# Optimization experiments

Measured on AMD Instinct MI355X. Metric: run time of the kernel, lower is better.

Reference implementation:

```python
import jax, jax.numpy as jnp
import numpy as np

B = 2
E = [16384, 32768, 65536, 131072]
CONVS = [256, 128, 64, 32, 8]


def mesh_conv(x, gemm, W, b):
    # x: (B, C, E); gemm: (E, 4) neighbor edge indices; W: (Cout, Cin, 5)
    n = x[:, :, gemm]  # (B, C, E, 4) irregular gather over mesh topology
    f1, f2, f3, f4 = n[..., 0], n[..., 1], n[..., 2], n[..., 3]
    # MeshCNN symmetric functions over the 4 gemm neighbors
    G = jnp.stack([x, f1 + f3, f2 + f4, jnp.abs(f1 - f3), jnp.abs(f2 - f4)], axis=-1)  # (B,C,E,5)
    return jnp.einsum('bces,ocs->boe', G, W) + b[None, :, None]


def inorm(x, eps=1e-5):
    # InstanceNorm2d, affine=False: normalize per (sample, channel) over edge dim
    m = jnp.mean(x, axis=2, keepdims=True)
    v = jnp.var(x, axis=2, keepdims=True)
    return (x - m) * jax.lax.rsqrt(v + eps)


def setup_inputs() -> dict:
    key = jax.random.key(0)
    ks = iter(jax.random.split(key, 64))
    inp = {}
    inp['fe'] = jax.random.normal(next(ks), (B, CONVS[0], E[0]), jnp.float32)
    for i in range(3):
        inp[f'skip{i}'] = jax.random.normal(next(ks), (B, CONVS[i + 1], E[i + 1]), jnp.float32)
    for r in range(4):
        inp[f'gemm{r}'] = jax.random.randint(next(ks), (E[r], 4), 0, E[r], jnp.int32)
    for i in range(3):
        inp[f'unpool{i}'] = jax.random.randint(next(ks), (E[i + 1],), 0, E[i], jnp.int32)

    def mk(cout, cin, name):
        inp[f'W{name}'] = jax.random.normal(next(ks), (cout, cin, 5), jnp.float32) * (1.0 / np.sqrt(5.0 * cin))
        inp[f'b{name}'] = jnp.zeros((cout,), jnp.float32)

    for i in range(3):
        mk(CONVS[i + 1], CONVS[i], f'up{i}')
        mk(CONVS[i + 1], CONVS[i + 1], f'c{i}')
    mk(CONVS[4], CONVS[3], 'upf')
    mk(CONVS[4], CONVS[4], 'cf')
    return inp


def reference(fe, skip0, skip1, skip2, gemm0, gemm1, gemm2, gemm3,
              unpool0, unpool1, unpool2,
              Wup0, bup0, Wc0, bc0, Wup1, bup1, Wc1, bc1, Wup2, bup2, Wc2, bc2,
              Wupf, bupf, Wcf, bcf):
    gemms = [gemm0, gemm1, gemm2, gemm3]
    unpools = [unpool0, unpool1, unpool2]
    skips = [skip0, skip1, skip2]
    Wups = [Wup0, Wup1, Wup2]
    bups = [bup0, bup1, bup2]
    Wcs = [Wc0, Wc1, Wc2]
    bcs = [bc0, bc1, bc2]
    x = fe
    for i in range(3):  # fixed small loop over decoder stages
        x1 = mesh_conv(x, gemms[i], Wups[i], bups[i])      # up_conv at coarse res
        x1 = x1[:, :, unpools[i]]                          # MeshUnpool: copy to fine edges
        x1 = x1 + skips[i]                                 # transfer_data skip add
        x1 = mesh_conv(x1, gemms[i + 1], Wcs[i], bcs[i])   # conv1 at fine res
        x = jax.nn.relu(inorm(x1))                         # InstanceNorm + ReLU (blocks=0)
    # final UpConv: no unroll, no skip
    x1 = mesh_conv(x, gemms[3], Wupf, bupf)
    x1 = mesh_conv(x1, gemms[3], Wcf, bcf)
    return jax.nn.relu(inorm(x1))
```

## Files before the change

kernel.cpp:

```cpp
#include <hip/hip_runtime.h>
#include <hip/hip_bf16.h>
#include <cstdint>
#include <cstddef>


typedef short s16x8 __attribute__((ext_vector_type(8)));
typedef float f32x4 __attribute__((ext_vector_type(4)));

__device__ __forceinline__ float bfbits2f(unsigned short u) {
    unsigned int x = ((unsigned int)u) << 16;
    float f; __builtin_memcpy(&f, &x, sizeof(f)); return f;
}
__device__ __forceinline__ unsigned short f2bfbits(float f) {
    __hip_bfloat16 h = __float2bfloat16(f);
    unsigned short u; __builtin_memcpy(&u, &h, sizeof(u)); return u;
}

__global__ __launch_bounds__(256) void k_transpose_in(
    const float* __restrict__ in, unsigned short* __restrict__ out, int C, int E)
{
    __shared__ float tile[64][65];
    const int e0 = blockIdx.x * 64;
    const int c0 = blockIdx.y * 64;
    const int b  = blockIdx.z;
    const float* inb = in + (size_t)b * C * E;
    const int l = threadIdx.x % 64;
    const int g = threadIdx.x / 64;
#pragma unroll
    for (int i = 0; i < 16; ++i) {
        const int c = i * 4 + g;
        tile[c][l] = inb[(size_t)(c0 + c) * E + e0 + l];
    }
    __syncthreads();
    unsigned short* outb = out + (size_t)b * E * C;
#pragma unroll
    for (int i = 0; i < 16; ++i) {
        const int e = i * 4 + g;
        outb[(size_t)(e0 + e) * C + c0 + l] = f2bfbits(tile[l][e]);
    }
}

__global__ __launch_bounds__(256) void k_prep_b(
    const float* __restrict__ W, unsigned short* __restrict__ Bp, int C, int O)
{
    const int p = blockIdx.x * 256 + threadIdx.x;
    const int total = 5 * C * O;
    if (p >= total) return;
    const int j = p & 7;
    const int t = p >> 3;
    const int o = t % O;
    const int kk = t / O;
    const int k = kk * 8 + j;
    const int s = k / C;
    const int c = k - s * C;
    Bp[p] = f2bfbits(W[((size_t)o * C + c) * 5 + s]);
}

__global__ __launch_bounds__(256) void k_prep_w(
    const float* __restrict__ W, float* __restrict__ Wt, int C, int O)
{
    const int idx = blockIdx.x * 256 + threadIdx.x;
    const int total = C * 5 * O;
    if (idx >= total) return;
    const int k = idx / O;
    const int o = idx % O;
    const int c = k / 5;
    const int s = k - 5 * c;
    Wt[idx] = W[((size_t)o * C + c) * 5 + s];
}

template<int C, int O>
__global__ __launch_bounds__(256) void k_conv_mfma(
    const unsigned short* __restrict__ x, const int* __restrict__ gm,
    const unsigned short* __restrict__ Bp, const float* __restrict__ bias,
    unsigned short* __restrict__ out, int E)
{
    constexpr int NT  = O / 16;
    constexpr int ITS = C / 32;
    static_assert(C % 32 == 0 && O % 16 == 0, "bad cfg");
    const int tid  = threadIdx.x;
    const int wave = tid >> 6;
    const int lane = tid & 63;
    const int m    = lane & 15;
    const int kq   = lane >> 4;
    const int b    = blockIdx.y;
    const int e    = blockIdx.x * 64 + wave * 16 + m;
    const unsigned short* xb = x + (size_t)b * E * C;

    const int4 gi = *reinterpret_cast<const int4*>(gm + 4 * (size_t)e);
    const unsigned short* p0  = xb + (size_t)e * C;
    const unsigned short* pf1 = xb + (size_t)gi.x * C;
    const unsigned short* pf2 = xb + (size_t)gi.y * C;
    const unsigned short* pf3 = xb + (size_t)gi.z * C;
    const unsigned short* pf4 = xb + (size_t)gi.w * C;

    const s16x8* Bp8 = reinterpret_cast<const s16x8*>(Bp);

    f32x4 acc[NT];
#pragma unroll
    for (int nt = 0; nt < NT; ++nt) acc[nt] = (f32x4){0.f, 0.f, 0.f, 0.f};

#pragma unroll
    for (int s = 0; s < 5; ++s) {
        const unsigned short* pa = (s == 0) ? p0 : ((s == 1 || s == 3) ? pf1 : pf2);
        const unsigned short* pb = (s == 0) ? p0 : ((s == 1 || s == 3) ? pf3 : pf4);
        for (int it = 0; it < ITS; ++it) {
            const int c0 = it * 32 + kq * 8;
            s16x8 afrag;
            if (s == 0) {
                afrag = *reinterpret_cast<const s16x8*>(pa + c0);
            } else {
                const s16x8 av = *reinterpret_cast<const s16x8*>(pa + c0);
                const s16x8 bv = *reinterpret_cast<const s16x8*>(pb + c0);
#pragma unroll
                for (int j = 0; j < 8; ++j) {
                    const float fa = bfbits2f((unsigned short)av[j]);
                    const float fb = bfbits2f((unsigned short)bv[j]);
                    const float t = (s < 3) ? (fa + fb) : fabsf(fa - fb);
                    afrag[j] = (short)f2bfbits(t);
                }
            }
            const int kk = s * (C / 8) + it * 4 + kq;
#pragma unroll
            for (int nt = 0; nt < NT; ++nt) {
                const s16x8 bfrag = Bp8[(size_t)kk * O + nt * 16 + m];
                acc[nt] = __builtin_amdgcn_mfma_f32_16x16x32_bf16(afrag, bfrag, acc[nt], 0, 0, 0);
            }
        }
    }

    const int ebase = blockIdx.x * 64 + wave * 16 + kq * 4;
#pragma unroll
    for (int nt = 0; nt < NT; ++nt) {
        const int o = nt * 16 + m;
        const float bo = bias[o];
#pragma unroll
        for (int r = 0; r < 4; ++r) {
            out[((size_t)b * E + (ebase + r)) * O + o] = f2bfbits(acc[nt][r] + bo);
        }
    }
}

template<int C, int O, int R_O, int R_E>
__global__ __launch_bounds__(256) void k_conv_small(
    const unsigned short* __restrict__ x, const int* __restrict__ gm,
    const float* __restrict__ Wt, const float* __restrict__ bias,
    unsigned short* __restrict__ out, int E)
{
    constexpr int OG = O / R_O;
    constexpr int EG = 256 / OG;
    constexpr int TILE_E = EG * R_E;
    static_assert(O % R_O == 0 && 256 % OG == 0, "bad cfg");
    const int tid = threadIdx.x;
    const int og  = tid % OG;
    const int eg  = tid / OG;
    const int b   = blockIdx.y;
    const int e0  = blockIdx.x * TILE_E + eg * R_E;
    const int o0  = og * R_O;
    const unsigned short* xb = x + (size_t)b * E * C;

    const unsigned short* rp[R_E][5];
#pragma unroll
    for (int j = 0; j < R_E; ++j) {
        const int e = e0 + j;
        const int4 gi = *reinterpret_cast<const int4*>(gm + 4 * (size_t)e);
        rp[j][0] = xb + (size_t)e * C;
        rp[j][1] = xb + (size_t)gi.x * C;
        rp[j][2] = xb + (size_t)gi.y * C;
        rp[j][3] = xb + (size_t)gi.z * C;
        rp[j][4] = xb + (size_t)gi.w * C;
    }

    float acc[R_E][R_O];
#pragma unroll
    for (int j = 0; j < R_E; ++j)
#pragma unroll
        for (int r = 0; r < R_O; ++r) acc[j][r] = 0.f;

    for (int c = 0; c < C; c += 4) {
        float xv[R_E][5][4];
#pragma unroll
        for (int j = 0; j < R_E; ++j)
#pragma unroll
            for (int k = 0; k < 5; ++k) {
                const ushort4 raw = *reinterpret_cast<const ushort4*>(rp[j][k] + c);
                xv[j][k][0] = bfbits2f(raw.x);
                xv[j][k][1] = bfbits2f(raw.y);
                xv[j][k][2] = bfbits2f(raw.z);
                xv[j][k][3] = bfbits2f(raw.w);
            }
#pragma unroll
        for (int cc = 0; cc < 4; ++cc) {
            float gv[R_E][5];
#pragma unroll
            for (int j = 0; j < R_E; ++j) {
                const float x0 = xv[j][0][cc];
                const float f1 = xv[j][1][cc];
                const float f2 = xv[j][2][cc];
                const float f3 = xv[j][3][cc];
                const float f4 = xv[j][4][cc];
                gv[j][0] = x0;
                gv[j][1] = f1 + f3;
                gv[j][2] = f2 + f4;
                gv[j][3] = fabsf(f1 - f3);
                gv[j][4] = fabsf(f2 - f4);
            }
            const float* wbase = Wt + ((size_t)(c + cc) * 5) * O + o0;
#pragma unroll
            for (int s = 0; s < 5; ++s) {
                const float4 wv = *reinterpret_cast<const float4*>(wbase + (size_t)s * O);
#pragma unroll
                for (int j = 0; j < R_E; ++j) {
                    acc[j][0] += gv[j][s] * wv.x;
                    acc[j][1] += gv[j][s] * wv.y;
                    acc[j][2] += gv[j][s] * wv.z;
                    acc[j][3] += gv[j][s] * wv.w;
                }
            }
        }
    }

#pragma unroll
    for (int j = 0; j < R_E; ++j) {
        ushort4 v;
        v.x = f2bfbits(acc[j][0] + bias[o0 + 0]);
        v.y = f2bfbits(acc[j][1] + bias[o0 + 1]);
        v.z = f2bfbits(acc[j][2] + bias[o0 + 2]);
        v.w = f2bfbits(acc[j][3] + bias[o0 + 3]);
        *reinterpret_cast<ushort4*>(out + ((size_t)b * E + (e0 + j)) * O + o0) = v;
    }
}

template<int O>
__global__ __launch_bounds__(256) void k_unpool_skip(
    const unsigned short* __restrict__ y, const int* __restrict__ up,
    const float* __restrict__ skip, unsigned short* __restrict__ out,
    int Ein, int Eout)
{
    const int b = blockIdx.y;
    const int idx = blockIdx.x * 256 + threadIdx.x;
    const int e = idx / O;
    const int o = idx % O;
    const int u = up[e];
    const float v = bfbits2f(y[((size_t)b * Ein + u) * O + o])
                  + skip[((size_t)b * O + o) * Eout + e];
    out[((size_t)b * Eout + e) * O + o] = f2bfbits(v);
}

template<int C>
__global__ __launch_bounds__(256) void k_stats(
    const unsigned short* __restrict__ x, float* __restrict__ stats, int E)
{
    constexpr int J = 256 / C;
    __shared__ float ssum[256];
    __shared__ float ssq[256];
    const int tid = threadIdx.x;
    const int c = tid % C;
    const int j = tid / C;
    const int b = blockIdx.y;
    const unsigned short* xb = x + ((size_t)b * E + (size_t)blockIdx.x * 256) * C;
    float s = 0.f, q = 0.f;
    for (int e = j; e < 256; e += J) {
        const float v = bfbits2f(xb[(size_t)e * C + c]);
        s += v; q += v * v;
    }
    ssum[tid] = s; ssq[tid] = q;
    __syncthreads();
    for (int st = 128; st >= C; st >>= 1) {
        if (tid < st) { ssum[tid] += ssum[tid + st]; ssq[tid] += ssq[tid + st]; }
        __syncthreads();
    }
    if (tid < C) {
        atomicAdd(&stats[((size_t)b * C + c) * 2], ssum[tid]);
        atomicAdd(&stats[((size_t)b * C + c) * 2 + 1], ssq[tid]);
    }
}

__global__ __launch_bounds__(256) void k_scale(
    const float* __restrict__ stats, float* __restrict__ ss, int BC, float invE)
{
    const int t = threadIdx.x;
    if (t < BC) {
        const float sum = stats[t * 2];
        const float sq  = stats[t * 2 + 1];
        const float m   = sum * invE;
        const float var = fmaxf(sq * invE - m * m, 0.f);
        const float sc  = rsqrtf(var + 1e-5f);
        ss[t * 2] = sc;
        ss[t * 2 + 1] = -m * sc;
    }
}

template<int C>
__global__ __launch_bounds__(256) void k_norm_relu(
    unsigned short* __restrict__ x, const float* __restrict__ ss, int E)
{
    const int b = blockIdx.y;
    const size_t idx = (size_t)blockIdx.x * 256 + threadIdx.x;
    const int c = (int)(idx % C);
    const float sc = ss[((size_t)b * C + c) * 2];
    const float sh = ss[((size_t)b * C + c) * 2 + 1];
    unsigned short* p = x + (size_t)b * E * C + idx;
    *p = f2bfbits(fmaxf(bfbits2f(*p) * sc + sh, 0.f));
}

__global__ __launch_bounds__(256) void k_final_out(
    const unsigned short* __restrict__ z, const float* __restrict__ ss,
    float* __restrict__ out, int E)
{
    const int b = blockIdx.y;
    const int idx = blockIdx.x * 256 + threadIdx.x;
    const int o = idx / E;
    const int e = idx % E;
    const float sc = ss[((size_t)b * 8 + o) * 2];
    const float sh = ss[((size_t)b * 8 + o) * 2 + 1];
    const float v = bfbits2f(z[((size_t)b * E + e) * 8 + o]) * sc + sh;
    out[(size_t)b * 8 * E + idx] = fmaxf(v, 0.f);
}

extern "C" void kernel_launch(void* const* d_in, const int* in_sizes, int n_in,
                              void* d_out, int out_size, void* d_ws, size_t ws_size,
                              hipStream_t stream)
{
    (void)in_sizes; (void)n_in; (void)out_size; (void)ws_size;

    const float* fe = (const float*)d_in[0];
    const int* gemm0 = (const int*)d_in[4];
    const int* gemm1 = (const int*)d_in[5];
    const int* gemm2 = (const int*)d_in[6];
    const int* gemm3 = (const int*)d_in[7];
    const int* up0 = (const int*)d_in[8];
    const int* up1 = (const int*)d_in[9];
    const int* up2 = (const int*)d_in[10];
    const float* bup0 = (const float*)d_in[12];
    const float* bc0  = (const float*)d_in[14];
    const float* bup1 = (const float*)d_in[16];
    const float* bc1  = (const float*)d_in[18];
    const float* bup2 = (const float*)d_in[20];
    const float* bc2  = (const float*)d_in[22];
    const float* bupf = (const float*)d_in[24];
    const float* bcf  = (const float*)d_in[26];

    unsigned short* wsb = (unsigned short*)d_ws;
    const size_t NP = 8388608;
    unsigned short* P0 = wsb;
    unsigned short* P1 = wsb + NP;
    unsigned short* P2 = wsb + 2 * NP;
    unsigned short* Bp_up0 = wsb + 3 * NP;
    unsigned short* Bp_c0  = Bp_up0 + 163840;
    unsigned short* Bp_up1 = Bp_c0  + 81920;
    unsigned short* Bp_c1  = Bp_up1 + 40960;
    unsigned short* Bp_up2 = Bp_c1  + 20480;
    unsigned short* Bp_c2  = Bp_up2 + 10240;
    float* fls    = (float*)(Bp_c2 + 5120);
    float* wt_upf = fls;
    float* wt_cf  = wt_upf + 1280;
    float* stats0 = wt_cf  + 320;
    float* stats1 = stats0 + 512;
    float* stats2 = stats1 + 256;
    float* stats3 = stats2 + 128;
    float* ss0    = stats3 + 32;
    float* ss1    = ss0 + 512;
    float* ss2    = ss1 + 256;
    float* ss3    = ss2 + 128;

    hipMemsetAsync(stats0, 0, 928 * sizeof(float), stream);

    const dim3 blk(256);

    k_transpose_in<<<dim3(16384 / 64, 256 / 64, 2), blk, 0, stream>>>(fe, P0, 256, 16384);

    k_prep_b<<<dim3(163840 / 256), blk, 0, stream>>>((const float*)d_in[11], Bp_up0, 256, 128);
    k_prep_b<<<dim3(81920 / 256),  blk, 0, stream>>>((const float*)d_in[13], Bp_c0, 128, 128);
    k_prep_b<<<dim3(40960 / 256),  blk, 0, stream>>>((const float*)d_in[15], Bp_up1, 128, 64);
    k_prep_b<<<dim3(20480 / 256),  blk, 0, stream>>>((const float*)d_in[17], Bp_c1, 64, 64);
    k_prep_b<<<dim3(10240 / 256),  blk, 0, stream>>>((const float*)d_in[19], Bp_up2, 64, 32);
    k_prep_b<<<dim3(5120 / 256),   blk, 0, stream>>>((const float*)d_in[21], Bp_c2, 32, 32);
    k_prep_w<<<dim3((1280 + 255) / 256), blk, 0, stream>>>((const float*)d_in[23], wt_upf, 32, 8);
    k_prep_w<<<dim3((320 + 255) / 256),  blk, 0, stream>>>((const float*)d_in[25], wt_cf, 8, 8);

    k_conv_mfma<256, 128><<<dim3(16384 / 64, 2), blk, 0, stream>>>(P0, gemm0, Bp_up0, bup0, P1, 16384);
    k_unpool_skip<128><<<dim3(32768 * 128 / 256, 2), blk, 0, stream>>>(P1, up0, (const float*)d_in[1], P2, 16384, 32768);
    k_conv_mfma<128, 128><<<dim3(32768 / 64, 2), blk, 0, stream>>>(P2, gemm1, Bp_c0, bc0, P0, 32768);
    k_stats<128><<<dim3(32768 / 256, 2), blk, 0, stream>>>(P0, stats0, 32768);
    k_scale<<<dim3(1), blk, 0, stream>>>(stats0, ss0, 256, 1.f / 32768.f);
    k_norm_relu<128><<<dim3(32768 * 128 / 256, 2), blk, 0, stream>>>(P0, ss0, 32768);

    k_conv_mfma<128, 64><<<dim3(32768 / 64, 2), blk, 0, stream>>>(P0, gemm1, Bp_up1, bup1, P1, 32768);
    k_unpool_skip<64><<<dim3(65536 * 64 / 256, 2), blk, 0, stream>>>(P1, up1, (const float*)d_in[2], P2, 32768, 65536);
    k_conv_mfma<64, 64><<<dim3(65536 / 64, 2), blk, 0, stream>>>(P2, gemm2, Bp_c1, bc1, P0, 65536);
    k_stats<64><<<dim3(65536 / 256, 2), blk, 0, stream>>>(P0, stats1, 65536);
    k_scale<<<dim3(1), blk, 0, stream>>>(stats1, ss1, 128, 1.f / 65536.f);
    k_norm_relu<64><<<dim3(65536 * 64 / 256, 2), blk, 0, stream>>>(P0, ss1, 65536);

    k_conv_mfma<64, 32><<<dim3(65536 / 64, 2), blk, 0, stream>>>(P0, gemm2, Bp_up2, bup2, P1, 65536);
    k_unpool_skip<32><<<dim3(131072 * 32 / 256, 2), blk, 0, stream>>>(P1, up2, (const float*)d_in[3], P2, 65536, 131072);
    k_conv_mfma<32, 32><<<dim3(131072 / 64, 2), blk, 0, stream>>>(P2, gemm3, Bp_c2, bc2, P0, 131072);
    k_stats<32><<<dim3(131072 / 256, 2), blk, 0, stream>>>(P0, stats2, 131072);
    k_scale<<<dim3(1), blk, 0, stream>>>(stats2, ss2, 64, 1.f / 131072.f);
    k_norm_relu<32><<<dim3(131072 * 32 / 256, 2), blk, 0, stream>>>(P0, ss2, 131072);

    k_conv_small<32, 8, 4, 2><<<dim3(131072 / 256, 2), blk, 0, stream>>>(P0, gemm3, wt_upf, bupf, P1, 131072);
    k_conv_small<8, 8, 4, 2><<<dim3(131072 / 256, 2), blk, 0, stream>>>(P1, gemm3, wt_cf, bcf, P2, 131072);
    k_stats<8><<<dim3(131072 / 256, 2), blk, 0, stream>>>(P2, stats3, 131072);
    k_scale<<<dim3(1), blk, 0, stream>>>(stats3, ss3, 16, 1.f / 131072.f);
    k_final_out<<<dim3(8 * 131072 / 256, 2), blk, 0, stream>>>(P2, ss3, (float*)d_out, 131072);
}
```

Before: 801.4 us.

## Fuse instance-norm stats into conv epilogues and vectorize unpool and norm kernels

Per-channel sum and sum-of-squares for instance norm are now accumulated in the conv epilogues (shuffles, shared memory, then atomics), which removes the separate stats kernels that re-read each conv output. The unpool+skip kernel now stages the channel-major skip tile through shared memory for coalesced float4 loads and writes ushort4, and norm_relu handles 8 bf16 values per thread. The small 8-output conv is rewritten so each thread owns one edge with all outputs and uses 16-byte gathers. Statistics are computed from fp32 pre-rounding values rather than the stored bf16, and atomic ordering makes them nondeterministic.

```diff
diff --git a/kernel.cpp b/kernel.cpp
--- a/kernel.cpp
+++ b/kernel.cpp
@@ -5,6 +5,7 @@
 
 
 typedef short s16x8 __attribute__((ext_vector_type(8)));
+typedef unsigned short u16x8 __attribute__((ext_vector_type(8)));
 typedef float f32x4 __attribute__((ext_vector_type(4)));
 
 __device__ __forceinline__ float bfbits2f(unsigned short u) {
@@ -69,11 +70,11 @@
     Wt[idx] = W[((size_t)o * C + c) * 5 + s];
 }
 
-template<int C, int O>
+template<int C, int O, bool STATS>
 __global__ __launch_bounds__(256) void k_conv_mfma(
     const unsigned short* __restrict__ x, const int* __restrict__ gm,
     const unsigned short* __restrict__ Bp, const float* __restrict__ bias,
-    unsigned short* __restrict__ out, int E)
+    unsigned short* __restrict__ out, float* __restrict__ stats, int E)
 {
     constexpr int NT  = O / 16;
     constexpr int ITS = C / 32;
@@ -130,104 +131,100 @@
     }
 
     const int ebase = blockIdx.x * 64 + wave * 16 + kq * 4;
+    float ssum[NT], ssq[NT];
 #pragma unroll
     for (int nt = 0; nt < NT; ++nt) {
         const int o = nt * 16 + m;
         const float bo = bias[o];
+        float s = 0.f, q = 0.f;
 #pragma unroll
         for (int r = 0; r < 4; ++r) {
-            out[((size_t)b * E + (ebase + r)) * O + o] = f2bfbits(acc[nt][r] + bo);
-        }
-    }
-}
-
-template<int C, int O, int R_O, int R_E>
+            const float z = acc[nt][r] + bo;
+            out[((size_t)b * E + (ebase + r)) * O + o] = f2bfbits(z);
+            s += z; q += z * z;
+        }
+        ssum[nt] = s; ssq[nt] = q;
+    }
+
+    if constexpr (STATS) {
+        __shared__ float ls[4][2][O];
+#pragma unroll
+        for (int nt = 0; nt < NT; ++nt) {
+            float s = ssum[nt], q = ssq[nt];
+            s += __shfl_xor(s, 16); s += __shfl_xor(s, 32);
+            q += __shfl_xor(q, 16); q += __shfl_xor(q, 32);
+            if (kq == 0) { ls[wave][0][nt * 16 + m] = s; ls[wave][1][nt * 16 + m] = q; }
+        }
+        __syncthreads();
+        if (tid < O) {
+            const float S = ls[0][0][tid] + ls[1][0][tid] + ls[2][0][tid] + ls[3][0][tid];
+            const float Q = ls[0][1][tid] + ls[1][1][tid] + ls[2][1][tid] + ls[3][1][tid];
+            atomicAdd(&stats[((size_t)b * O + tid) * 2], S);
+            atomicAdd(&stats[((size_t)b * O + tid) * 2 + 1], Q);
+        }
+    }
+}
+
+template<int C, int O, bool STATS>
 __global__ __launch_bounds__(256) void k_conv_small(
     const unsigned short* __restrict__ x, const int* __restrict__ gm,
     const float* __restrict__ Wt, const float* __restrict__ bias,
-    unsigned short* __restrict__ out, int E)
-{
-    constexpr int OG = O / R_O;
-    constexpr int EG = 256 / OG;
-    constexpr int TILE_E = EG * R_E;
-    static_assert(O % R_O == 0 && 256 % OG == 0, "bad cfg");
+    unsigned short* __restrict__ out, float* __restrict__ stats, int E)
+{
+    static_assert(O == 8 && C % 8 == 0, "bad cfg");
+    __shared__ float ls[2 * O];
     const int tid = threadIdx.x;
-    const int og  = tid % OG;
-    const int eg  = tid / OG;
-    const int b   = blockIdx.y;
-    const int e0  = blockIdx.x * TILE_E + eg * R_E;
-    const int o0  = og * R_O;
+    if constexpr (STATS) {
+        if (tid < 2 * O) ls[tid] = 0.f;
+        __syncthreads();
+    }
+    const int b = blockIdx.y;
+    const int e = blockIdx.x * 256 + tid;
     const unsigned short* xb = x + (size_t)b * E * C;
-
-    const unsigned short* rp[R_E][5];
-#pragma unroll
-    for (int j = 0; j < R_E; ++j) {
-        const int e = e0 + j;
-        const int4 gi = *reinterpret_cast<const int4*>(gm + 4 * (size_t)e);
-        rp[j][0] = xb + (size_t)e * C;
-        rp[j][1] = xb + (size_t)gi.x * C;
-        rp[j][2] = xb + (size_t)gi.y * C;
-        rp[j][3] = xb + (size_t)gi.z * C;
-        rp[j][4] = xb + (size_t)gi.w * C;
-    }
-
-    float acc[R_E][R_O];
-#pragma unroll
-    for (int j = 0; j < R_E; ++j)
-#pragma unroll
-        for (int r = 0; r < R_O; ++r) acc[j][r] = 0.f;
-
-    for (int c = 0; c < C; c += 4) {
-        float xv[R_E][5][4];
-#pragma unroll
-        for (int j = 0; j < R_E; ++j)
-#pragma unroll
-            for (int k = 0; k < 5; ++k) {
-                const ushort4 raw = *reinterpret_cast<const ushort4*>(rp[j][k] + c);
-                xv[j][k][0] = bfbits2f(raw.x);
-                xv[j][k][1] = bfbits2f(raw.y);
-                xv[j][k][2] = bfbits2f(raw.z);
-                xv[j][k][3] = bfbits2f(raw.w);
-            }
-#pragma unroll
-        for (int cc = 0; cc < 4; ++cc) {
-            float gv[R_E][5];
-#pragma unroll
-            for (int j = 0; j < R_E; ++j) {
-                const float x0 = xv[j][0][cc];
-                const float f1 = xv[j][1][cc];
-                const float f2 = xv[j][2][cc];
-                const float f3 = xv[j][3][cc];
-                const float f4 = xv[j][4][cc];
-                gv[j][0] = x0;
-                gv[j][1] = f1 + f3;
-                gv[j][2] = f2 + f4;
-                gv[j][3] = fabsf(f1 - f3);
-                gv[j][4] = fabsf(f2 - f4);
-            }
-            const float* wbase = Wt + ((size_t)(c + cc) * 5) * O + o0;
-#pragma unroll
-            for (int s = 0; s < 5; ++s) {
-                const float4 wv = *reinterpret_cast<const float4*>(wbase + (size_t)s * O);
-#pragma unroll
-                for (int j = 0; j < R_E; ++j) {
-                    acc[j][0] += gv[j][s] * wv.x;
-                    acc[j][1] += gv[j][s] * wv.y;
-                    acc[j][2] += gv[j][s] * wv.z;
-                    acc[j][3] += gv[j][s] * wv.w;
-                }
-            }
-        }
-    }
-
-#pragma unroll
-    for (int j = 0; j < R_E; ++j) {
-        ushort4 v;
-        v.x = f2bfbits(acc[j][0] + bias[o0 + 0]);
-        v.y = f2bfbits(acc[j][1] + bias[o0 + 1]);
-        v.z = f2bfbits(acc[j][2] + bias[o0 + 2]);
-        v.w = f2bfbits(acc[j][3] + bias[o0 + 3]);
-        *reinterpret_cast<ushort4*>(out + ((size_t)b * E + (e0 + j)) * O + o0) = v;
+    const int4 gi = *reinterpret_cast<const int4*>(gm + 4 * (size_t)e);
+    const unsigned short* rp[5] = {
+        xb + (size_t)e * C, xb + (size_t)gi.x * C, xb + (size_t)gi.y * C,
+        xb + (size_t)gi.z * C, xb + (size_t)gi.w * C };
+
+    float acc[O];
+#pragma unroll
+    for (int o = 0; o < O; ++o) acc[o] = bias[o];
+
+#pragma unroll
+    for (int c = 0; c < C; c += 8) {
+        u16x8 rv[5];
+#pragma unroll
+        for (int k = 0; k < 5; ++k) rv[k] = *reinterpret_cast<const u16x8*>(rp[k] + c);
+#pragma unroll
+        for (int cc = 0; cc < 8; ++cc) {
+            const float x0 = bfbits2f(rv[0][cc]);
+            const float f1 = bfbits2f(rv[1][cc]);
+            const float f2 = bfbits2f(rv[2][cc]);
+            const float f3 = bfbits2f(rv[3][cc]);
+            const float f4 = bfbits2f(rv[4][cc]);
+            const float gv[5] = { x0, f1 + f3, f2 + f4, fabsf(f1 - f3), fabsf(f2 - f4) };
+            const float* wbase = Wt + (size_t)(c + cc) * 5 * O;
+#pragma unroll
+            for (int s = 0; s < 5; ++s)
+#pragma unroll
+                for (int o = 0; o < O; ++o)
+                    acc[o] += gv[s] * wbase[s * O + o];
+        }
+    }
+
+    u16x8 ov;
+#pragma unroll
+    for (int o = 0; o < O; ++o) ov[o] = f2bfbits(acc[o]);
+    *reinterpret_cast<u16x8*>(out + ((size_t)b * E + e) * O) = ov;
+
+    if constexpr (STATS) {
+#pragma unroll
+        for (int o = 0; o < O; ++o) {
+            atomicAdd(&ls[o * 2], acc[o]);
+            atomicAdd(&ls[o * 2 + 1], acc[o] * acc[o]);
+        }
+        __syncthreads();
+        if (tid < 2 * O) atomicAdd(&stats[(size_t)b * 2 * O + tid], ls[tid]);
     }
 }
 
@@ -237,42 +234,41 @@
     const float* __restrict__ skip, unsigned short* __restrict__ out,
     int Ein, int Eout)
 {
-    const int b = blockIdx.y;
-    const int idx = blockIdx.x * 256 + threadIdx.x;
-    const int e = idx / O;
-    const int o = idx % O;
-    const int u = up[e];
-    const float v = bfbits2f(y[((size_t)b * Ein + u) * O + o])
-                  + skip[((size_t)b * O + o) * Eout + e];
-    out[((size_t)b * Eout + e) * O + o] = f2bfbits(v);
-}
-
-template<int C>
-__global__ __launch_bounds__(256) void k_stats(
-    const unsigned short* __restrict__ x, float* __restrict__ stats, int E)
-{
-    constexpr int J = 256 / C;
-    __shared__ float ssum[256];
-    __shared__ float ssq[256];
-    const int tid = threadIdx.x;
-    const int c = tid % C;
-    const int j = tid / C;
-    const int b = blockIdx.y;
-    const unsigned short* xb = x + ((size_t)b * E + (size_t)blockIdx.x * 256) * C;
-    float s = 0.f, q = 0.f;
-    for (int e = j; e < 256; e += J) {
-        const float v = bfbits2f(xb[(size_t)e * C + c]);
-        s += v; q += v * v;
-    }
-    ssum[tid] = s; ssq[tid] = q;
+    __shared__ float sk[O][65];
+    const int b  = blockIdx.y;
+    const int e0 = blockIdx.x * 64;
+    const int t  = threadIdx.x;
+    constexpr int L = O / 16;
+#pragma unroll
+    for (int i = 0; i < L; ++i) {
+        const int flat = i * 256 + t;
+        const int o = flat >> 4;
+        const int el4 = (flat & 15) * 4;
+        const float4 v = *reinterpret_cast<const float4*>(
+            skip + ((size_t)b * O + o) * Eout + e0 + el4);
+        sk[o][el4]     = v.x;
+        sk[o][el4 + 1] = v.y;
+        sk[o][el4 + 2] = v.z;
+        sk[o][el4 + 3] = v.w;
+    }
     __syncthreads();
-    for (int st = 128; st >= C; st >>= 1) {
-        if (tid < st) { ssum[tid] += ssum[tid + st]; ssq[tid] += ssq[tid + st]; }
-        __syncthreads();
-    }
-    if (tid < C) {
-        atomicAdd(&stats[((size_t)b * C + c) * 2], ssum[tid]);
-        atomicAdd(&stats[((size_t)b * C + c) * 2 + 1], ssq[tid]);
+    constexpr int OG  = O / 4;
+    constexpr int EPP = 256 / OG;
+    const int o4  = (t % OG) * 4;
+    const int elg = t / OG;
+#pragma unroll
+    for (int p = 0; p < 64 / EPP; ++p) {
+        const int el = p * EPP + elg;
+        const int e  = e0 + el;
+        const int u  = up[e];
+        const ushort4 yv = *reinterpret_cast<const ushort4*>(
+            y + ((size_t)b * Ein + u) * O + o4);
+        ushort4 ov;
+        ov.x = f2bfbits(bfbits2f(yv.x) + sk[o4 + 0][el]);
+        ov.y = f2bfbits(bfbits2f(yv.y) + sk[o4 + 1][el]);
+        ov.z = f2bfbits(bfbits2f(yv.z) + sk[o4 + 2][el]);
+        ov.w = f2bfbits(bfbits2f(yv.w) + sk[o4 + 3][el]);
+        *reinterpret_cast<ushort4*>(out + ((size_t)b * Eout + e) * O + o4) = ov;
     }
 }
 
@@ -296,12 +292,18 @@
     unsigned short* __restrict__ x, const float* __restrict__ ss, int E)
 {
     const int b = blockIdx.y;
-    const size_t idx = (size_t)blockIdx.x * 256 + threadIdx.x;
-    const int c = (int)(idx % C);
-    const float sc = ss[((size_t)b * C + c) * 2];
-    const float sh = ss[((size_t)b * C + c) * 2 + 1];
-    unsigned short* p = x + (size_t)b * E * C + idx;
-    *p = f2bfbits(fmaxf(bfbits2f(*p) * sc + sh, 0.f));
+    const size_t i8 = ((size_t)blockIdx.x * 256 + threadIdx.x) * 8;
+    const int c0 = (int)(i8 % C);
+    unsigned short* p = x + (size_t)b * E * C + i8;
+    const u16x8 v = *reinterpret_cast<const u16x8*>(p);
+    u16x8 r;
+#pragma unroll
+    for (int j = 0; j < 8; ++j) {
+        const float sc = ss[(b * C + c0 + j) * 2];
+        const float sh = ss[(b * C + c0 + j) * 2 + 1];
+        r[j] = f2bfbits(fmaxf(bfbits2f(v[j]) * sc + sh, 0.f));
+    }
+    *reinterpret_cast<u16x8*>(p) = r;
 }
 
 __global__ __launch_bounds__(256) void k_final_out(
@@ -379,30 +381,26 @@
     k_prep_w<<<dim3((1280 + 255) / 256), blk, 0, stream>>>((const float*)d_in[23], wt_upf, 32, 8);
     k_prep_w<<<dim3((320 + 255) / 256),  blk, 0, stream>>>((const float*)d_in[25], wt_cf, 8, 8);
 
-    k_conv_mfma<256, 128><<<dim3(16384 / 64, 2), blk, 0, stream>>>(P0, gemm0, Bp_up0, bup0, P1, 16384);
-    k_unpool_skip<128><<<dim3(32768 * 128 / 256, 2), blk, 0, stream>>>(P1, up0, (const float*)d_in[1], P2, 16384, 32768);
-    k_conv_mfma<128, 128><<<dim3(32768 / 64, 2), blk, 0, stream>>>(P2, gemm1, Bp_c0, bc0, P0, 32768);
-    k_stats<128><<<dim3(32768 / 256, 2), blk, 0, stream>>>(P0, stats0, 32768);
+    k_conv_mfma<256, 128, false><<<dim3(16384 / 64, 2), blk, 0, stream>>>(P0, gemm0, Bp_up0, bup0, P1, nullptr, 16384);
+    k_unpool_skip<128><<<dim3(32768 / 64, 2), blk, 0, stream>>>(P1, up0, (const float*)d_in[1], P2, 16384, 32768);
+    k_conv_mfma<128, 128, true><<<dim3(32768 / 64, 2), blk, 0, stream>>>(P2, gemm1, Bp_c0, bc0, P0, stats0, 32768);
     k_scale<<<dim3(1), blk, 0, stream>>>(stats0, ss0, 256, 1.f / 32768.f);
-    k_norm_relu<128><<<dim3(32768 * 128 / 256, 2), blk, 0, stream>>>(P0, ss0, 32768);
-
-    k_conv_mfma<128, 64><<<dim3(32768 / 64, 2), blk, 0, stream>>>(P0, gemm1, Bp_up1, bup1, P1, 32768);
-    k_unpool_skip<64><<<dim3(65536 * 64 / 256, 2), blk, 0, stream>>>(P1, up1, (const float*)d_in[2], P2, 32768, 65536);
-    k_conv_mfma<64, 64><<<dim3(65536 / 64, 2), blk, 0, stream>>>(P2, gemm2, Bp_c1, bc1, P0, 65536);
-    k_stats<64><<<dim3(65536 / 256, 2), blk, 0, stream>>>(P0, stats1, 65536);
+    k_norm_relu<128><<<dim3(32768 * 128 / 2048, 2), blk, 0, stream>>>(P0, ss0, 32768);
+
+    k_conv_mfma<128, 64, false><<<dim3(32768 / 64, 2), blk, 0, stream>>>(P0, gemm1, Bp_up1, bup1, P1, nullptr, 32768);
+    k_unpool_skip<64><<<dim3(65536 / 64, 2), blk, 0, stream>>>(P1, up1, (const float*)d_in[2], P2, 32768, 65536);
+    k_conv_mfma<64, 64, true><<<dim3(65536 / 64, 2), blk, 0, stream>>>(P2, gemm2, Bp_c1, bc1, P0, stats1, 65536);
     k_scale<<<dim3(1), blk, 0, stream>>>(stats1, ss1, 128, 1.f / 65536.f);
-    k_norm_relu<64><<<dim3(65536 * 64 / 256, 2), blk, 0, stream>>>(P0, ss1, 65536);
-
-    k_conv_mfma<64, 32><<<dim3(65536 / 64, 2), blk, 0, stream>>>(P0, gemm2, Bp_up2, bup2, P1, 65536);
-    k_unpool_skip<32><<<dim3(131072 * 32 / 256, 2), blk, 0, stream>>>(P1, up2, (const float*)d_in[3], P2, 65536, 131072);
-    k_conv_mfma<32, 32><<<dim3(131072 / 64, 2), blk, 0, stream>>>(P2, gemm3, Bp_c2, bc2, P0, 131072);
-    k_stats<32><<<dim3(131072 / 256, 2), blk, 0, stream>>>(P0, stats2, 131072);
+    k_norm_relu<64><<<dim3(65536 * 64 / 2048, 2), blk, 0, stream>>>(P0, ss1, 65536);
+
+    k_conv_mfma<64, 32, false><<<dim3(65536 / 64, 2), blk, 0, stream>>>(P0, gemm2, Bp_up2, bup2, P1, nullptr, 65536);
+    k_unpool_skip<32><<<dim3(131072 / 64, 2), blk, 0, stream>>>(P1, up2, (const float*)d_in[3], P2, 65536, 131072);
+    k_conv_mfma<32, 32, true><<<dim3(131072 / 64, 2), blk, 0, stream>>>(P2, gemm3, Bp_c2, bc2, P0, stats2, 131072);
     k_scale<<<dim3(1), blk, 0, stream>>>(stats2, ss2, 64, 1.f / 131072.f);
-    k_norm_relu<32><<<dim3(131072 * 32 / 256, 2), blk, 0, stream>>>(P0, ss2, 131072);
-
-    k_conv_small<32, 8, 4, 2><<<dim3(131072 / 256, 2), blk, 0, stream>>>(P0, gemm3, wt_upf, bupf, P1, 131072);
-    k_conv_small<8, 8, 4, 2><<<dim3(131072 / 256, 2), blk, 0, stream>>>(P1, gemm3, wt_cf, bcf, P2, 131072);
-    k_stats<8><<<dim3(131072 / 256, 2), blk, 0, stream>>>(P2, stats3, 131072);
+    k_norm_relu<32><<<dim3(131072 * 32 / 2048, 2), blk, 0, stream>>>(P0, ss2, 131072);
+
+    k_conv_small<32, 8, false><<<dim3(131072 / 256, 2), blk, 0, stream>>>(P0, gemm3, wt_upf, bupf, P1, nullptr, 131072);
+    k_conv_small<8, 8, true><<<dim3(131072 / 256, 2), blk, 0, stream>>>(P1, gemm3, wt_cf, bcf, P2, stats3, 131072);
     k_scale<<<dim3(1), blk, 0, stream>>>(stats3, ss3, 16, 1.f / 131072.f);
     k_final_out<<<dim3(8 * 131072 / 256, 2), blk, 0, stream>>>(P2, ss3, (float*)d_out, 131072);
 }
```

New measurement: 785.7 us. No clear change (-2.0%).
